# Performance work log

Measured on AMD Instinct MI355X. Metric: run time of the kernel, lower is better.

The kernel has to match this reference:

```python
import jax, jax.numpy as jnp
import numpy as np

B, D, O = 8192, 64, 256

def setup_inputs() -> dict:
    key = jax.random.key(0)
    k1, k2, k3 = jax.random.split(key, 3)
    x = jax.random.normal(k1, (B, D), dtype=jnp.float32)
    centers = jax.random.uniform(k2, (O, 1, D), dtype=jnp.float32)  # RandomUniform(0,1)
    # Original uses Constant(10.0) which saturates exp(-quad) to 0; use small random
    # betas so the quadratic form is in a numerically meaningful range.
    betas = jax.random.normal(k3, (O, D, D), dtype=jnp.float32) * 0.05
    return {"x": x, "centers": centers, "betas": betas}

def reference(x, centers, betas):
    # precision[o] = betas[o] @ betas[o]^T   -> [O, D, D]
    precision = jnp.einsum('ode,ofe->odf', betas, betas)
    # diff[o,b,:] = centers[o] - x[b]        -> [O, B, D]
    diff = centers - x[None, :, :]
    # quad[o,b] = diff[o,b]^T P[o] diff[o,b] -> [O, B]
    quad = jnp.einsum('obd,odf,obf->ob', diff, precision, diff)
    return jnp.exp(-quad).T  # [B, O]
```

## Files before the change

kernel.cpp:

```cpp
#include <hip/hip_runtime.h>
#include <hip/hip_bf16.h>

typedef __bf16 bf16x8 __attribute__((ext_vector_type(8)));
typedef float  f32x4  __attribute__((ext_vector_type(4)));
typedef float  f32x16 __attribute__((ext_vector_type(16)));

constexpr int Bn = 8192, Dn = 64, On = 256;

#define GLD16(g, l) __builtin_amdgcn_global_load_lds( \
    (const __attribute__((address_space(1))) void*)(g), \
    (__attribute__((address_space(3))) void*)(l), 16, 0, 0)

__global__ void k_prep(const float* __restrict__ betas, const float* __restrict__ centers,
                       __bf16* __restrict__ bTsw, float* __restrict__ ncpk) {
    __shared__ float s[64 * 65];
    const int o = blockIdx.x, tid = threadIdx.x;
    const float* bo = betas + (size_t)o * 4096;
    for (int j = tid; j < 1024; j += 256) {
        int d = j >> 4, e4 = (j & 15) * 4;
        float4 v = ((const float4*)bo)[j];
        s[d * 65 + e4 + 0] = v.x; s[d * 65 + e4 + 1] = v.y;
        s[d * 65 + e4 + 2] = v.z; s[d * 65 + e4 + 3] = v.w;
    }
    __syncthreads();
    for (int p = tid; p < 4096; p += 256) {
        int chunk = p >> 3, j = p & 7;
        int ek = chunk >> 6, lane = chunk & 63;
        int e = (ek >> 2) * 32 + (lane & 31);
        int d = ((ek & 3) * 2 + (lane >> 5)) * 8 + j;
        bTsw[(size_t)o * 4096 + p] = (__bf16)s[d * 65 + e];
    }
    if (tid < 64) {
        int et = tid >> 5, rem = tid & 31, l5 = rem >> 4, reg = rem & 15;
        int row = et * 32 + l5 * 4 + (reg & 3) + ((reg >> 2) << 3);
        float acc = 0.f;
        for (int d = 0; d < 64; ++d) acc += s[d * 65 + row] * centers[o * 64 + d];
        ncpk[o * 64 + tid] = -acc;
    }
}

__global__ void __launch_bounds__(256)
__attribute__((amdgpu_waves_per_eu(2, 2)))
k_main(const float* __restrict__ x, const __bf16* __restrict__ bTsw,
       const float* __restrict__ ncpk, float* __restrict__ out) {
    __shared__ __align__(16) unsigned char smem[2 * 8192 + 2048];
    __bf16* sA0 = (__bf16*)smem;
    __bf16* sA1 = (__bf16*)(smem + 8192);
    float*  sCp = (float*)(smem + 16384);

    const int tid = threadIdx.x, wq = tid >> 6, lane = tid & 63;
    const int l31 = lane & 31, l5 = lane >> 5;
    const int bbase = blockIdx.x * 512;
    const int o0 = blockIdx.y * 8;

    sCp[tid]       = ncpk[o0 * 64 + tid];
    sCp[256 + tid] = ncpk[o0 * 64 + 256 + tid];

    bf16x8 xf[4][4];
#pragma unroll
    for (int bt = 0; bt < 4; ++bt)
#pragma unroll
        for (int kk = 0; kk < 4; ++kk) {
            const float* xp = x + (size_t)(bbase + wq * 128 + bt * 32 + l31) * 64
                                + (kk * 2 + l5) * 8;
            float4 v0 = *(const float4*)xp, v1 = *(const float4*)(xp + 4);
            bf16x8 f;
            f[0] = (__bf16)v0.x; f[1] = (__bf16)v0.y; f[2] = (__bf16)v0.z; f[3] = (__bf16)v0.w;
            f[4] = (__bf16)v1.x; f[5] = (__bf16)v1.y; f[6] = (__bf16)v1.z; f[7] = (__bf16)v1.w;
            xf[bt][kk] = f;
        }

    auto prefetch = [&](int o, __bf16* buf) {
        const __bf16* g = bTsw + (size_t)o * 4096;
        GLD16(g + (size_t)(wq * 128 + lane) * 8,      buf + (wq * 128) * 8);
        GLD16(g + (size_t)(wq * 128 + 64 + lane) * 8, buf + (wq * 128 + 64) * 8);
    };

    float qd[16];
    prefetch(o0, sA0);
    __builtin_amdgcn_s_waitcnt(0x0f70);
    __syncthreads();

#pragma unroll
    for (int oi = 0; oi < 8; ++oi) {
        __bf16* cur = (oi & 1) ? sA1 : sA0;
        if (oi < 7) prefetch(o0 + oi + 1, (oi & 1) ? sA0 : sA1);

        f32x4 qv[4] = {{0,0,0,0},{0,0,0,0},{0,0,0,0},{0,0,0,0}};
#pragma unroll
        for (int et = 0; et < 2; ++et) {
            f32x16 cpv;
#pragma unroll
            for (int r4 = 0; r4 < 4; ++r4)
                ((f32x4*)&cpv)[r4] = *(const f32x4*)(sCp + oi * 64 + et * 32 + l5 * 16 + r4 * 4);
            bf16x8 af[4];
#pragma unroll
            for (int k = 0; k < 4; ++k)
                af[k] = *(const bf16x8*)(cur + (size_t)((et * 4 + k) * 64 + lane) * 8);
#pragma unroll
            for (int bt = 0; bt < 4; ++bt) {
                f32x16 acc = __builtin_amdgcn_mfma_f32_32x32x16_bf16(af[0], xf[bt][0], cpv, 0, 0, 0);
                acc = __builtin_amdgcn_mfma_f32_32x32x16_bf16(af[1], xf[bt][1], acc, 0, 0, 0);
                acc = __builtin_amdgcn_mfma_f32_32x32x16_bf16(af[2], xf[bt][2], acc, 0, 0, 0);
                acc = __builtin_amdgcn_mfma_f32_32x32x16_bf16(af[3], xf[bt][3], acc, 0, 0, 0);
                const f32x4* aq = (const f32x4*)&acc;
                qv[bt] += aq[0] * aq[0];
                qv[bt] += aq[1] * aq[1];
                qv[bt] += aq[2] * aq[2];
                qv[bt] += aq[3] * aq[3];
            }
        }
        float q[4];
#pragma unroll
        for (int bt = 0; bt < 4; ++bt) {
            float qs = (qv[bt][0] + qv[bt][1]) + (qv[bt][2] + qv[bt][3]);
            qs += __shfl_xor(qs, 32, 64);
            q[bt] = qs;
        }
        qd[oi * 2 + 0] = l5 ? q[2] : q[0];
        qd[oi * 2 + 1] = l5 ? q[3] : q[1];

        __builtin_amdgcn_sched_barrier(0);
        __builtin_amdgcn_s_waitcnt(0x0f70);
        __syncthreads();
    }

    float* scr = (float*)smem + wq * 1152;
#pragma unroll
    for (int oi = 0; oi < 8; ++oi) {
        scr[(l5 * 64 + l31) * 9 + oi]      = qd[oi * 2 + 0];
        scr[(l5 * 64 + 32 + l31) * 9 + oi] = qd[oi * 2 + 1];
    }
    __syncthreads();
#pragma unroll
    for (int rr = 0; rr < 2; ++rr) {
        int r = lane * 2 + rr;
        const float* q8 = scr + r * 9;
        f32x4 r0, r1;
#pragma unroll
        for (int j = 0; j < 4; ++j) { r0[j] = __expf(-q8[j]); r1[j] = __expf(-q8[4 + j]); }
        float* op = out + (size_t)(bbase + wq * 128 + r) * 256 + o0;
        *(f32x4*)op       = r0;
        *(f32x4*)(op + 4) = r1;
    }
}

extern "C" void kernel_launch(void* const* d_in, const int* in_sizes, int n_in,
                              void* d_out, int out_size, void* d_ws, size_t ws_size,
                              hipStream_t stream) {
    const float* x       = (const float*)d_in[0];
    const float* centers = (const float*)d_in[1];
    const float* betas   = (const float*)d_in[2];
    float* out = (float*)d_out;

    char* ws = (char*)d_ws;
    __bf16* bTsw = (__bf16*)ws;
    float*  ncpk = (float*)(ws + 2 * (1 << 20));

    k_prep<<<dim3(On),                dim3(256), 0, stream>>>(betas, centers, bTsw, ncpk);
    k_main<<<dim3(Bn / 512, On / 8),  dim3(256), 0, stream>>>(x, bTsw, ncpk, out);
}
```

Measured before the change: 87.52 us.

## Halve per-block batch tile to 256 rows and raise occupancy target

Each wave now handles 64 batch rows instead of 128, so the grid doubles to 32x32 blocks and per-thread register arrays shrink (x fragments, accumulators, results). The waves_per_eu(2,2) cap is replaced with launch_bounds(256,4) to allow more resident waves, and the epilogue is rewritten so each thread writes one output row from a padded LDS scratch using vector loads. The aim is more latency hiding and better CU fill. In exchange, each staged betas tile is reused across fewer batch rows, which doubles global/LDS traffic for betas per unit of work.

```diff
diff --git a/kernel.cpp b/kernel.cpp
--- a/kernel.cpp
+++ b/kernel.cpp
@@ -39,8 +39,7 @@
     }
 }
 
-__global__ void __launch_bounds__(256)
-__attribute__((amdgpu_waves_per_eu(2, 2)))
+__global__ void __launch_bounds__(256, 4)
 k_main(const float* __restrict__ x, const __bf16* __restrict__ bTsw,
        const float* __restrict__ ncpk, float* __restrict__ out) {
     __shared__ __align__(16) unsigned char smem[2 * 8192 + 2048];
@@ -50,18 +49,18 @@
 
     const int tid = threadIdx.x, wq = tid >> 6, lane = tid & 63;
     const int l31 = lane & 31, l5 = lane >> 5;
-    const int bbase = blockIdx.x * 512;
+    const int bbase = blockIdx.x * 256;
     const int o0 = blockIdx.y * 8;
 
     sCp[tid]       = ncpk[o0 * 64 + tid];
     sCp[256 + tid] = ncpk[o0 * 64 + 256 + tid];
 
-    bf16x8 xf[4][4];
+    bf16x8 xf[2][4];
 #pragma unroll
-    for (int bt = 0; bt < 4; ++bt)
+    for (int bt = 0; bt < 2; ++bt)
 #pragma unroll
         for (int kk = 0; kk < 4; ++kk) {
-            const float* xp = x + (size_t)(bbase + wq * 128 + bt * 32 + l31) * 64
+            const float* xp = x + (size_t)(bbase + wq * 64 + bt * 32 + l31) * 64
                                 + (kk * 2 + l5) * 8;
             float4 v0 = *(const float4*)xp, v1 = *(const float4*)(xp + 4);
             bf16x8 f;
@@ -76,7 +75,7 @@
         GLD16(g + (size_t)(wq * 128 + 64 + lane) * 8, buf + (wq * 128 + 64) * 8);
     };
 
-    float qd[16];
+    float qd[8];
     prefetch(o0, sA0);
     __builtin_amdgcn_s_waitcnt(0x0f70);
     __syncthreads();
@@ -86,7 +85,7 @@
         __bf16* cur = (oi & 1) ? sA1 : sA0;
         if (oi < 7) prefetch(o0 + oi + 1, (oi & 1) ? sA0 : sA1);
 
-        f32x4 qv[4] = {{0,0,0,0},{0,0,0,0},{0,0,0,0},{0,0,0,0}};
+        f32x4 qv[2] = {{0,0,0,0},{0,0,0,0}};
 #pragma unroll
         for (int et = 0; et < 2; ++et) {
             f32x16 cpv;
@@ -98,7 +97,7 @@
             for (int k = 0; k < 4; ++k)
                 af[k] = *(const bf16x8*)(cur + (size_t)((et * 4 + k) * 64 + lane) * 8);
 #pragma unroll
-            for (int bt = 0; bt < 4; ++bt) {
+            for (int bt = 0; bt < 2; ++bt) {
                 f32x16 acc = __builtin_amdgcn_mfma_f32_32x32x16_bf16(af[0], xf[bt][0], cpv, 0, 0, 0);
                 acc = __builtin_amdgcn_mfma_f32_32x32x16_bf16(af[1], xf[bt][1], acc, 0, 0, 0);
                 acc = __builtin_amdgcn_mfma_f32_32x32x16_bf16(af[2], xf[bt][2], acc, 0, 0, 0);
@@ -110,38 +109,34 @@
                 qv[bt] += aq[3] * aq[3];
             }
         }
-        float q[4];
-#pragma unroll
-        for (int bt = 0; bt < 4; ++bt) {
-            float qs = (qv[bt][0] + qv[bt][1]) + (qv[bt][2] + qv[bt][3]);
-            qs += __shfl_xor(qs, 32, 64);
-            q[bt] = qs;
-        }
-        qd[oi * 2 + 0] = l5 ? q[2] : q[0];
-        qd[oi * 2 + 1] = l5 ? q[3] : q[1];
+        float q0 = (qv[0][0] + qv[0][1]) + (qv[0][2] + qv[0][3]);
+        float q1 = (qv[1][0] + qv[1][1]) + (qv[1][2] + qv[1][3]);
+        q0 += __shfl_xor(q0, 32, 64);
+        q1 += __shfl_xor(q1, 32, 64);
+        qd[oi] = l5 ? q1 : q0;
 
         __builtin_amdgcn_sched_barrier(0);
         __builtin_amdgcn_s_waitcnt(0x0f70);
         __syncthreads();
     }
+    __syncthreads();
 
-    float* scr = (float*)smem + wq * 1152;
+    float* scr = (float*)smem;
+    {
+        int r = wq * 64 + l5 * 32 + l31;
 #pragma unroll
-    for (int oi = 0; oi < 8; ++oi) {
-        scr[(l5 * 64 + l31) * 9 + oi]      = qd[oi * 2 + 0];
-        scr[(l5 * 64 + 32 + l31) * 9 + oi] = qd[oi * 2 + 1];
+        for (int oi = 0; oi < 8; ++oi) scr[r * 12 + oi] = qd[oi];
     }
     __syncthreads();
+    {
+        const float* q8 = scr + tid * 12;
+        f32x4 r0 = *(const f32x4*)q8, r1 = *(const f32x4*)(q8 + 4);
+        f32x4 e0, e1;
 #pragma unroll
-    for (int rr = 0; rr < 2; ++rr) {
-        int r = lane * 2 + rr;
-        const float* q8 = scr + r * 9;
-        f32x4 r0, r1;
-#pragma unroll
-        for (int j = 0; j < 4; ++j) { r0[j] = __expf(-q8[j]); r1[j] = __expf(-q8[4 + j]); }
-        float* op = out + (size_t)(bbase + wq * 128 + r) * 256 + o0;
-        *(f32x4*)op       = r0;
-        *(f32x4*)(op + 4) = r1;
+        for (int j = 0; j < 4; ++j) { e0[j] = __expf(-r0[j]); e1[j] = __expf(-r1[j]); }
+        float* op = out + (size_t)(bbase + tid) * 256 + o0;
+        *(f32x4*)op       = e0;
+        *(f32x4*)(op + 4) = e1;
     }
 }
 
@@ -158,5 +153,5 @@
     float*  ncpk = (float*)(ws + 2 * (1 << 20));
 
     k_prep<<<dim3(On),                dim3(256), 0, stream>>>(betas, centers, bTsw, ncpk);
-    k_main<<<dim3(Bn / 512, On / 8),  dim3(256), 0, stream>>>(x, bTsw, ncpk, out);
+    k_main<<<dim3(Bn / 256, On / 8),  dim3(256), 0, stream>>>(x, bTsw, ncpk, out);
 }
```

Measured after the change: 89.00 us. About the same (+1.7%).
